# Performance work log

Hardware: AMD Instinct MI355X
Metric: run time of the kernel (lower is better)

The kernel has to match this reference:

```python
import jax, jax.numpy as jnp
import numpy as np

B, C, H, W = 2, 512, 64, 64


def conv1x1(x, w, b):
    # x: [B,C,H,W], w: [O,C], b: [O]
    return jnp.einsum('bchw,oc->bohw', x, w) + b[None, :, None, None]


def setup_inputs() -> dict:
    key = jax.random.key(0)
    ks = jax.random.split(key, 20)
    d = {
        'visSegF': jax.random.normal(ks[0], (B, C, H, W), jnp.float32),
        'irSegF': jax.random.normal(ks[1], (B, C, H, W), jnp.float32),
        'x_vis_p': jax.random.normal(ks[2], (B, C, H, W), jnp.float32),
        'x_ir_p': jax.random.normal(ks[3], (B, C, H, W), jnp.float32),
    }
    names = ['q_rd', 'k_rd', 'v_rd', 'q_dr', 'k_dr', 'v_dr']
    for i, n in enumerate(names):
        d['W' + n] = jax.random.normal(ks[4 + 2 * i], (C, C), jnp.float32) * 0.02
        d['b' + n] = jax.random.normal(ks[5 + 2 * i], (C,), jnp.float32) * 0.01
    # gamma params are init-zero in torch; use small nonzero values so both paths contribute
    d['gamma_rd'] = jax.random.normal(ks[16], (1,), jnp.float32) * 0.1
    d['gamma_dr'] = jax.random.normal(ks[17], (1,), jnp.float32) * 0.1
    return d


def reference(visSegF, irSegF, x_vis_p, x_ir_p,
              Wq_rd, bq_rd, Wk_rd, bk_rd, Wv_rd, bv_rd,
              Wq_dr, bq_dr, Wk_dr, bk_dr, Wv_dr, bv_dr,
              gamma_rd, gamma_dr):
    b, c, h, w = x_vis_p.shape
    n = h * w

    # rd path: query from x_vis_p, key from visSegF, value from x_ir_p (sr_ratio == 1 branch)
    q_vis = conv1x1(x_vis_p, Wq_rd, bq_rd).reshape(b, c, n)      # [B,C,N]
    key_d = conv1x1(visSegF, Wk_rd, bk_rd).reshape(b, c, -1)     # [B,C,M]
    val_d = conv1x1(x_ir_p, Wv_rd, bv_rd).reshape(b, c, -1)      # [B,C,M]
    # torch: softmax(bmm(q^T, k), dim=1) -> softmax over query positions (axis=1)
    attn_rd = jax.nn.softmax(jnp.einsum('bcn,bcm->bnm', q_vis, key_d), axis=1)
    out_rd = jnp.einsum('bcm,bnm->bcn', val_d, attn_rd).reshape(b, c, h, w)

    # dr path: query from x_ir_p, key/value from irSegF
    q_ir = conv1x1(x_ir_p, Wq_dr, bq_dr).reshape(b, c, n)
    key_r = conv1x1(irSegF, Wk_dr, bk_dr).reshape(b, c, -1)
    val_r = conv1x1(irSegF, Wv_dr, bv_dr).reshape(b, c, -1)
    attn_dr = jax.nn.softmax(jnp.einsum('bcn,bcm->bnm', q_ir, key_r), axis=1)
    out_dr = jnp.einsum('bcm,bnm->bcn', val_r, attn_dr).reshape(b, c, h, w)

    out_rd = jax.nn.relu(gamma_rd[0] * out_rd + x_vis_p)
    out_dr = jax.nn.relu(gamma_dr[0] * out_dr + x_ir_p)
    return (out_rd, out_dr)
```

## Files before the change

### kernel.cpp

```cpp
#include <hip/hip_runtime.h>
#include <stdint.h>


typedef __attribute__((ext_vector_type(8))) __bf16 bf16x8;
typedef __attribute__((ext_vector_type(4))) float f32x4;

__device__ __forceinline__ unsigned short f2bf(float f) {
  union { float f; unsigned u; } v; v.f = f;
  unsigned r = v.u + 0x7FFFu + ((v.u >> 16) & 1u);
  return (unsigned short)(r >> 16);
}
__device__ __forceinline__ float bf2f(unsigned short b) {
  union { unsigned u; float f; } v; v.u = ((unsigned)b) << 16;
  return v.f;
}

__device__ __forceinline__ void async_copy16(const unsigned short* g,
                                             unsigned short* l) {
  __builtin_amdgcn_global_load_lds(
      (const __attribute__((address_space(1))) unsigned int*)g,
      (__attribute__((address_space(3))) unsigned int*)l, 16, 0, 0);
}

template <int NSUB>
__device__ __forceinline__ void gemm_core(
    const unsigned short* __restrict__ Ag, const unsigned short* __restrict__ Bg,
    int K, int lda, int ldb, int rowbase, int colbase,
    f32x4 (&acc)[4][4], unsigned short* Al, unsigned short* Bl) {
  const int tid = threadIdx.x;
  const int w = tid >> 6, lane = tid & 63;
  const int quad = lane >> 4, l16 = lane & 15;
  const int wm = (w >> 1) << 6, wn = (w & 1) << 6;
  const int rbase = (w << 5) + (lane >> 2);

  for (int k0 = 0; k0 < K; k0 += 32 * NSUB) {
#pragma unroll
    for (int half = 0; half < NSUB; ++half) {
      int kh = k0 + (half << 5);
      unsigned short* Ah = Al + (half << 12);
      unsigned short* Bh = Bl + (half << 12);
#pragma unroll
      for (int i = 0; i < 2; ++i) {
        int rloc = rbase + (i << 4);
        int cg = (lane & 3) ^ ((rloc >> 1) & 3);
        int koff = kh + (cg << 3);
        int ldsoff = ((w << 5) + (i << 4)) << 5;
        async_copy16(Ag + (size_t)(rowbase + rloc) * lda + koff, Ah + ldsoff);
        async_copy16(Bg + (size_t)(colbase + rloc) * ldb + koff, Bh + ldsoff);
      }
    }
    __syncthreads();
#pragma unroll
    for (int half = 0; half < NSUB; ++half) {
      unsigned short* Ah = Al + (half << 12);
      unsigned short* Bh = Bl + (half << 12);
      bf16x8 af[4], bfr[4];
#pragma unroll
      for (int i = 0; i < 4; ++i) {
        int r = wm + (i << 4) + l16;
        af[i] = *(const bf16x8*)(Ah + (r << 5) + ((quad ^ ((r >> 1) & 3)) << 3));
      }
#pragma unroll
      for (int j = 0; j < 4; ++j) {
        int r = wn + (j << 4) + l16;
        bfr[j] = *(const bf16x8*)(Bh + (r << 5) + ((quad ^ ((r >> 1) & 3)) << 3));
      }
#pragma unroll
      for (int i = 0; i < 4; ++i)
#pragma unroll
        for (int j = 0; j < 4; ++j)
          acc[i][j] = __builtin_amdgcn_mfma_f32_16x16x32_bf16(af[i], bfr[j], acc[i][j], 0, 0, 0);
    }
    __syncthreads();
  }
}

struct WArgs { const float* src[6]; unsigned short* dst[6]; };
__global__ __launch_bounds__(256) void k_cvtw(WArgs a) {
  int z = blockIdx.y;
  int i = blockIdx.x * 256 + threadIdx.x;
  a.dst[z][i] = f2bf(a.src[z][i]);
}

struct TArgs { const float* src[4]; unsigned short* dst[4]; };
__global__ __launch_bounds__(256) void k_tcvt(TArgs a) {
  __shared__ float tile[32][33];
  const float* src = a.src[blockIdx.z];
  unsigned short* dst = a.dst[blockIdx.z];
  int n0 = blockIdx.x << 5;
  int r0 = blockIdx.y << 5;
  int tx = threadIdx.x & 31, ty = threadIdx.x >> 5;
#pragma unroll
  for (int i = 0; i < 4; ++i)
    tile[ty * 4 + i][tx] = src[(size_t)(r0 + ty * 4 + i) * 4096 + n0 + tx];
  __syncthreads();
  int b = r0 >> 9, c0 = r0 & 511;
#pragma unroll
  for (int i = 0; i < 4; ++i) {
    int nn = ty * 4 + i;
    dst[(size_t)b * (4096 * 512) + (size_t)(n0 + nn) * 512 + c0 + tx] =
        f2bf(tile[tx][nn]);
  }
}

struct ConvArgs {
  const unsigned short* W[12];
  const unsigned short* X[12];
  const float* bias[12];
  unsigned short* out[12];
  int trans[12];
};
__global__ __launch_bounds__(256) void k_conv(ConvArgs a) {
  __shared__ unsigned short sh[16384];
  int z = blockIdx.z;
  int trans = a.trans[z];
  int rowbase = (trans ? blockIdx.x : blockIdx.y) << 7;
  int colbase = (trans ? blockIdx.y : blockIdx.x) << 7;
  const unsigned short* Ag = trans ? a.X[z] : a.W[z];
  const unsigned short* Bg = trans ? a.W[z] : a.X[z];
  f32x4 acc[4][4];
#pragma unroll
  for (int i = 0; i < 4; ++i)
#pragma unroll
    for (int j = 0; j < 4; ++j) acc[i][j] = (f32x4){0.f, 0.f, 0.f, 0.f};
  gemm_core<2>(Ag, Bg, 512, 512, 512, rowbase, colbase, acc, sh, sh + 8192);

  const int tid = threadIdx.x, w = tid >> 6, lane = tid & 63;
  const int quad = lane >> 4, l16 = lane & 15;
  const int wm = (w >> 1) << 6, wn = (w & 1) << 6;
  const float* bias = a.bias[z];
  unsigned short* out = a.out[z];
  if (trans) {
    float bo[4];
#pragma unroll
    for (int j = 0; j < 4; ++j) bo[j] = bias[colbase + wn + (j << 4) + l16];
#pragma unroll
    for (int i = 0; i < 4; ++i) {
      int n0 = rowbase + wm + (i << 4) + (quad << 2);
#pragma unroll
      for (int j = 0; j < 4; ++j) {
        int o = colbase + wn + (j << 4) + l16;
        out[(size_t)(n0 + 0) * 512 + o] = f2bf(acc[i][j].x + bo[j]);
        out[(size_t)(n0 + 1) * 512 + o] = f2bf(acc[i][j].y + bo[j]);
        out[(size_t)(n0 + 2) * 512 + o] = f2bf(acc[i][j].z + bo[j]);
        out[(size_t)(n0 + 3) * 512 + o] = f2bf(acc[i][j].w + bo[j]);
      }
    }
  } else {
#pragma unroll
    for (int i = 0; i < 4; ++i) {
      int o0 = rowbase + wm + (i << 4) + (quad << 2);
      float b0 = bias[o0], b1 = bias[o0 + 1], b2 = bias[o0 + 2], b3 = bias[o0 + 3];
#pragma unroll
      for (int j = 0; j < 4; ++j) {
        int n = colbase + wn + (j << 4) + l16;
        out[(size_t)(o0 + 0) * 4096 + n] = f2bf(acc[i][j].x + b0);
        out[(size_t)(o0 + 1) * 4096 + n] = f2bf(acc[i][j].y + b1);
        out[(size_t)(o0 + 2) * 4096 + n] = f2bf(acc[i][j].z + b2);
        out[(size_t)(o0 + 3) * 4096 + n] = f2bf(acc[i][j].w + b3);
      }
    }
  }
}

struct QKArgs {
  const unsigned short* Q[4]; const unsigned short* K[4]; unsigned short* T[4];
  float* pz;
};
__global__ __launch_bounds__(256) void k_qk(QKArgs a) {
  __shared__ unsigned short sh[16384];
  int z = blockIdx.z;
  int nbase = blockIdx.y << 7;
  int mbase = blockIdx.x << 7;
  f32x4 acc[4][4];
#pragma unroll
  for (int i = 0; i < 4; ++i)
#pragma unroll
    for (int j = 0; j < 4; ++j) acc[i][j] = (f32x4){0.f, 0.f, 0.f, 0.f};
  gemm_core<2>(a.Q[z], a.K[z], 512, 512, 512, nbase, mbase, acc, sh, sh + 8192);

  const int tid = threadIdx.x, w = tid >> 6, lane = tid & 63;
  const int quad = lane >> 4, l16 = lane & 15;
  const int wm = (w >> 1) << 6, wn = (w & 1) << 6;
  unsigned short* T = a.T[z];
  float sjv[4] = {0.f, 0.f, 0.f, 0.f};
#pragma unroll
  for (int i = 0; i < 4; ++i) {
    int n0 = nbase + wm + (i << 4) + (quad << 2);
#pragma unroll
    for (int j = 0; j < 4; ++j) {
      int m = mbase + wn + (j << 4) + l16;
      float e0 = __expf(acc[i][j].x);
      float e1 = __expf(acc[i][j].y);
      float e2 = __expf(acc[i][j].z);
      float e3 = __expf(acc[i][j].w);
      T[(size_t)(n0 + 0) * 4096 + m] = f2bf(e0);
      T[(size_t)(n0 + 1) * 4096 + m] = f2bf(e1);
      T[(size_t)(n0 + 2) * 4096 + m] = f2bf(e2);
      T[(size_t)(n0 + 3) * 4096 + m] = f2bf(e3);
      sjv[j] += e0 + e1 + e2 + e3;
    }
  }
  float* red = (float*)sh;
#pragma unroll
  for (int j = 0; j < 4; ++j) {
    float s = sjv[j];
    s += __shfl_xor(s, 16, 64);
    s += __shfl_xor(s, 32, 64);
    if (quad == 0) red[(w << 6) + (j << 4) + l16] = s;
  }
  __syncthreads();
  if (tid < 128) {
    int h = tid >> 6, t = tid & 63;
    float S = red[(h << 6) + t] + red[((h + 2) << 6) + t];
    int m = mbase + (h << 6) + t;
    a.pz[((z << 5) + blockIdx.y) * 4096 + m] = S;
  }
}

__global__ __launch_bounds__(256) void k_stats2(const float* __restrict__ pz,
                                                float* __restrict__ c) {
  int m = (blockIdx.x << 8) + threadIdx.x;
  int z = blockIdx.y;
  float S = 0.f;
#pragma unroll
  for (int k = 0; k < 32; ++k) S += pz[((z << 5) + k) * 4096 + m];
  c[z * 4096 + m] = 1.f / S;
}

struct VSArgs { unsigned short* V[4]; const float* c; };
__global__ __launch_bounds__(256) void k_vscale(VSArgs a) {
  int z = blockIdx.y;
  int t = blockIdx.x * 256 + threadIdx.x;
  int m0 = (t & 511) << 3;
  int row = t >> 9;
  unsigned short* p = a.V[z] + (size_t)row * 4096 + m0;
  const float* cz = a.c + z * 4096 + m0;
  int4 raw = *(const int4*)p;
  unsigned short* u = (unsigned short*)&raw;
#pragma unroll
  for (int j = 0; j < 8; ++j) u[j] = f2bf(bf2f(u[j]) * cz[j]);
  *(int4*)p = raw;
}

struct PVArgs {
  const unsigned short* V[4];
  const unsigned short* P[4];
  const float* resid[4];
  const float* gamma[4];
  float* out[4];
};
__global__ __launch_bounds__(256) void k_pv(PVArgs a) {
  __shared__ unsigned short sh[32768];
  int z = blockIdx.z;
  int rowbase = blockIdx.y << 7;
  int colbase = blockIdx.x << 7;
  f32x4 acc[4][4];
#pragma unroll
  for (int i = 0; i < 4; ++i)
#pragma unroll
    for (int j = 0; j < 4; ++j) acc[i][j] = (f32x4){0.f, 0.f, 0.f, 0.f};
  gemm_core<4>(a.V[z], a.P[z], 4096, 4096, 4096, rowbase, colbase, acc, sh, sh + 16384);

  const int tid = threadIdx.x, w = tid >> 6, lane = tid & 63;
  const int quad = lane >> 4, l16 = lane & 15;
  const int wm = (w >> 1) << 6, wn = (w & 1) << 6;
  float g = a.gamma[z][0];
  const float* R = a.resid[z];
  float* O = a.out[z];
#pragma unroll
  for (int i = 0; i < 4; ++i) {
    int c0 = rowbase + wm + (i << 4) + (quad << 2);
#pragma unroll
    for (int j = 0; j < 4; ++j) {
      int n = colbase + wn + (j << 4) + l16;
      O[(size_t)(c0 + 0) * 4096 + n] = fmaxf(g * acc[i][j].x + R[(size_t)(c0 + 0) * 4096 + n], 0.f);
      O[(size_t)(c0 + 1) * 4096 + n] = fmaxf(g * acc[i][j].y + R[(size_t)(c0 + 1) * 4096 + n], 0.f);
      O[(size_t)(c0 + 2) * 4096 + n] = fmaxf(g * acc[i][j].z + R[(size_t)(c0 + 2) * 4096 + n], 0.f);
      O[(size_t)(c0 + 3) * 4096 + n] = fmaxf(g * acc[i][j].w + R[(size_t)(c0 + 3) * 4096 + n], 0.f);
    }
  }
}

extern "C" void kernel_launch(void* const* d_in, const int* in_sizes, int n_in,
                              void* d_out, int out_size, void* d_ws, size_t ws_size,
                              hipStream_t stream) {
  char* ws = (char*)d_ws;
  unsigned short* wb  = (unsigned short*)(ws);
  unsigned short* xt  = (unsigned short*)(ws + 3145728);
  unsigned short* qkv = (unsigned short*)(ws + 36700160);
  unsigned short* tt  = (unsigned short*)(ws + 87031808);
  float* pz  = (float*)(ws + 3145728);
  float* cb  = (float*)(ws + 3145728 + 2097152);

  WArgs wa;
  for (int i = 0; i < 6; ++i) {
    wa.src[i] = (const float*)d_in[4 + 2 * i];
    wa.dst[i] = wb + (size_t)i * 262144;
  }
  k_cvtw<<<dim3(1024, 6), 256, 0, stream>>>(wa);

  TArgs ta;
  for (int ai = 0; ai < 4; ++ai) {
    ta.src[ai] = (const float*)d_in[ai];
    ta.dst[ai] = xt + (size_t)ai * 4194304;
  }
  k_tcvt<<<dim3(128, 32, 4), 256, 0, stream>>>(ta);

  const int srcArr[6] = {2, 0, 3, 3, 1, 1};
  const int trans[6] = {1, 1, 0, 1, 1, 0};
  ConvArgs ca;
  for (int ci = 0; ci < 6; ++ci)
    for (int b = 0; b < 2; ++b) {
      int zz = ci * 2 + b;
      ca.W[zz] = wb + (size_t)ci * 262144;
      ca.X[zz] = xt + (size_t)srcArr[ci] * 4194304 + (size_t)b * 2097152;
      ca.bias[zz] = (const float*)d_in[5 + 2 * ci];
      ca.out[zz] = qkv + (size_t)zz * 2097152;
      ca.trans[zz] = trans[ci];
    }
  k_conv<<<dim3(32, 4, 12), 256, 0, stream>>>(ca);

  QKArgs qa;
  for (int path = 0; path < 2; ++path)
    for (int b = 0; b < 2; ++b) {
      int zz = path * 2 + b;
      qa.Q[zz] = qkv + (size_t)((path * 3 + 0) * 2 + b) * 2097152;
      qa.K[zz] = qkv + (size_t)((path * 3 + 1) * 2 + b) * 2097152;
      qa.T[zz] = tt + (size_t)zz * 16777216;
    }
  qa.pz = pz;
  k_qk<<<dim3(32, 32, 4), 256, 0, stream>>>(qa);

  k_stats2<<<dim3(16, 4), 256, 0, stream>>>(pz, cb);

  VSArgs va;
  for (int path = 0; path < 2; ++path)
    for (int b = 0; b < 2; ++b)
      va.V[path * 2 + b] = qkv + (size_t)((path * 3 + 2) * 2 + b) * 2097152;
  va.c = cb;
  k_vscale<<<dim3(1024, 4), 256, 0, stream>>>(va);

  PVArgs pa;
  const float* resid_src[2] = {(const float*)d_in[2], (const float*)d_in[3]};
  const float* gsrc[2] = {(const float*)d_in[16], (const float*)d_in[17]};
  for (int path = 0; path < 2; ++path)
    for (int b = 0; b < 2; ++b) {
      int zz = path * 2 + b;
      pa.V[zz] = qkv + (size_t)((path * 3 + 2) * 2 + b) * 2097152;
      pa.P[zz] = tt + (size_t)zz * 16777216;
      pa.resid[zz] = resid_src[path] + (size_t)b * 2097152;
      pa.gamma[zz] = gsrc[path];
      pa.out[zz] = (float*)d_out + (size_t)path * 4194304 + (size_t)b * 2097152;
    }
  k_pv<<<dim3(32, 4, 4), 256, 0, stream>>>(pa);
}
```

Baseline: 399.8 us.

## Split PV GEMM along K into two halves with separate reduction epilogue kernel

```diff
diff --git a/kernel.cpp b/kernel.cpp
--- a/kernel.cpp
+++ b/kernel.cpp
@@ -246,40 +246,59 @@
 struct PVArgs {
   const unsigned short* V[4];
   const unsigned short* P[4];
+  float* part[8];
+};
+__global__ __launch_bounds__(256) void k_pv(PVArgs a) {
+  __shared__ unsigned short sh[16384];
+  int zk = blockIdx.z;
+  int z = zk & 3, kc = zk >> 2;
+  int rowbase = blockIdx.y << 7;
+  int colbase = blockIdx.x << 7;
+  f32x4 acc[4][4];
+#pragma unroll
+  for (int i = 0; i < 4; ++i)
+#pragma unroll
+    for (int j = 0; j < 4; ++j) acc[i][j] = (f32x4){0.f, 0.f, 0.f, 0.f};
+  gemm_core<2>(a.V[z] + (kc << 11), a.P[z] + (kc << 11), 2048, 4096, 4096,
+               rowbase, colbase, acc, sh, sh + 8192);
+
+  const int tid = threadIdx.x, w = tid >> 6, lane = tid & 63;
+  const int quad = lane >> 4, l16 = lane & 15;
+  const int wm = (w >> 1) << 6, wn = (w & 1) << 6;
+  float* O = a.part[zk];
+#pragma unroll
+  for (int i = 0; i < 4; ++i) {
+    int c0 = rowbase + wm + (i << 4) + (quad << 2);
+#pragma unroll
+    for (int j = 0; j < 4; ++j) {
+      int n = colbase + wn + (j << 4) + l16;
+      O[(size_t)(c0 + 0) * 4096 + n] = acc[i][j].x;
+      O[(size_t)(c0 + 1) * 4096 + n] = acc[i][j].y;
+      O[(size_t)(c0 + 2) * 4096 + n] = acc[i][j].z;
+      O[(size_t)(c0 + 3) * 4096 + n] = acc[i][j].w;
+    }
+  }
+}
+
+struct RedArgs {
+  const float* p1[4];
   const float* resid[4];
   const float* gamma[4];
   float* out[4];
 };
-__global__ __launch_bounds__(256) void k_pv(PVArgs a) {
-  __shared__ unsigned short sh[32768];
-  int z = blockIdx.z;
-  int rowbase = blockIdx.y << 7;
-  int colbase = blockIdx.x << 7;
-  f32x4 acc[4][4];
-#pragma unroll
-  for (int i = 0; i < 4; ++i)
-#pragma unroll
-    for (int j = 0; j < 4; ++j) acc[i][j] = (f32x4){0.f, 0.f, 0.f, 0.f};
-  gemm_core<4>(a.V[z], a.P[z], 4096, 4096, 4096, rowbase, colbase, acc, sh, sh + 16384);
-
-  const int tid = threadIdx.x, w = tid >> 6, lane = tid & 63;
-  const int quad = lane >> 4, l16 = lane & 15;
-  const int wm = (w >> 1) << 6, wn = (w & 1) << 6;
+__global__ __launch_bounds__(256) void k_red(RedArgs a) {
+  int z = blockIdx.y;
+  size_t i = ((size_t)blockIdx.x * 256 + threadIdx.x) << 2;
+  float4 v0 = *(const float4*)(a.out[z] + i);
+  float4 v1 = *(const float4*)(a.p1[z] + i);
+  float4 r  = *(const float4*)(a.resid[z] + i);
   float g = a.gamma[z][0];
-  const float* R = a.resid[z];
-  float* O = a.out[z];
-#pragma unroll
-  for (int i = 0; i < 4; ++i) {
-    int c0 = rowbase + wm + (i << 4) + (quad << 2);
-#pragma unroll
-    for (int j = 0; j < 4; ++j) {
-      int n = colbase + wn + (j << 4) + l16;
-      O[(size_t)(c0 + 0) * 4096 + n] = fmaxf(g * acc[i][j].x + R[(size_t)(c0 + 0) * 4096 + n], 0.f);
-      O[(size_t)(c0 + 1) * 4096 + n] = fmaxf(g * acc[i][j].y + R[(size_t)(c0 + 1) * 4096 + n], 0.f);
-      O[(size_t)(c0 + 2) * 4096 + n] = fmaxf(g * acc[i][j].z + R[(size_t)(c0 + 2) * 4096 + n], 0.f);
-      O[(size_t)(c0 + 3) * 4096 + n] = fmaxf(g * acc[i][j].w + R[(size_t)(c0 + 3) * 4096 + n], 0.f);
-    }
-  }
+  float4 o;
+  o.x = fmaxf(g * (v0.x + v1.x) + r.x, 0.f);
+  o.y = fmaxf(g * (v0.y + v1.y) + r.y, 0.f);
+  o.z = fmaxf(g * (v0.z + v1.z) + r.z, 0.f);
+  o.w = fmaxf(g * (v0.w + v1.w) + r.w, 0.f);
+  *(float4*)(a.out[z] + i) = o;
 }
 
 extern "C" void kernel_launch(void* const* d_in, const int* in_sizes, int n_in,
@@ -342,16 +361,31 @@
   k_vscale<<<dim3(1024, 4), 256, 0, stream>>>(va);
 
   PVArgs pa;
+  float* p1base[4] = {
+      (float*)(qkv + (size_t)0 * 2097152),
+      (float*)(qkv + (size_t)2 * 2097152),
+      (float*)(qkv + (size_t)6 * 2097152),
+      (float*)(qkv + (size_t)8 * 2097152)};
+  for (int path = 0; path < 2; ++path)
+    for (int b = 0; b < 2; ++b) {
+      int zz = path * 2 + b;
+      pa.V[zz] = qkv + (size_t)((path * 3 + 2) * 2 + b) * 2097152;
+      pa.P[zz] = tt + (size_t)zz * 16777216;
+      pa.part[zz] = (float*)d_out + (size_t)zz * 2097152;
+      pa.part[4 + zz] = p1base[zz];
+    }
+  k_pv<<<dim3(32, 4, 8), 256, 0, stream>>>(pa);
+
+  RedArgs ra;
   const float* resid_src[2] = {(const float*)d_in[2], (const float*)d_in[3]};
   const float* gsrc[2] = {(const float*)d_in[16], (const float*)d_in[17]};
   for (int path = 0; path < 2; ++path)
     for (int b = 0; b < 2; ++b) {
       int zz = path * 2 + b;
-      pa.V[zz] = qkv + (size_t)((path * 3 + 2) * 2 + b) * 2097152;
-      pa.P[zz] = tt + (size_t)zz * 16777216;
-      pa.resid[zz] = resid_src[path] + (size_t)b * 2097152;
-      pa.gamma[zz] = gsrc[path];
-      pa.out[zz] = (float*)d_out + (size_t)path * 4194304 + (size_t)b * 2097152;
-    }
-  k_pv<<<dim3(32, 4, 4), 256, 0, stream>>>(pa);
-}
+      ra.p1[zz] = p1base[zz];
+      ra.resid[zz] = resid_src[path] + (size_t)b * 2097152;
+      ra.gamma[zz] = gsrc[path];
+      ra.out[zz] = (float*)d_out + (size_t)zz * 2097152;
+    }
+  k_red<<<dim3(2048, 4), 256, 0, stream>>>(ra);
+}
```

Measured after the change: 413.0 us. 1.03x slower.
